# Optimization experiments

Measured on AMD Instinct MI355X. Metric: run time of the kernel, lower is better.

## Reference

```python
import jax, jax.numpy as jnp
import numpy as np

INF = 1e9  # large additive-mask constant (original code's INF)
D_KEY = 64


def setup_inputs() -> dict:
    key = jax.random.key(0)
    kq, kk, kv = jax.random.split(key, 3)
    B, S, D = 8, 2048, 64
    return {
        "query": jax.random.normal(kq, (B, S, D), dtype=jnp.float32),
        "key": jax.random.normal(kk, (B, S, D), dtype=jnp.float32),
        "value": jax.random.normal(kv, (B, S, D), dtype=jnp.float32),
    }


def reference(query, key, value):
    # scores: [B, Sq, Sk]
    scores = jnp.einsum("bqd,bkd->bqk", query, key)
    Sk = key.shape[1]
    # strict upper-triangular additive causal mask, subtracted BEFORE scaling
    tri = jnp.triu(jnp.ones((Sk, Sk), dtype=scores.dtype), k=1) * INF
    scores = scores - tri[None, :, :]
    scale = jnp.asarray(np.sqrt(D_KEY), dtype=scores.dtype)
    attn = jax.nn.softmax(scores / scale, axis=2)  # dropout ratio = 0.0
    return jnp.einsum("bqk,bkd->bqd", attn, value)
```

## Files before the change

### kernel.cpp

```cpp
#include <hip/hip_runtime.h>
#include <hip/hip_bf16.h>

typedef __attribute__((ext_vector_type(8))) short bf16x8;
typedef __attribute__((ext_vector_type(4))) float f32x4;
typedef __attribute__((ext_vector_type(4))) unsigned short us4;

#define BATCH 8
#define SEQ 2048
#define DIM 64
#define QB 64
#define NQT 32
#define NKT 32
#define TE 4096
#define CH 4
#define CPB 144
#define QSCALE (0.125f * 1.44269504088896f)
#define THR 8.0f

__device__ __forceinline__ unsigned short f2bf(float f) {
    return __builtin_bit_cast(unsigned short, __float2bfloat16(f));
}

__device__ __forceinline__ int kswz(int row, int d) {
    return (row * DIM + d) ^ ((row & 7) << 3);
}
__device__ __forceinline__ int vswz(int d, int kv) {
    return (d * 64 + kv) ^ ((((d & 7) ^ ((d >> 2) & 7)) & 7) << 3);
}
__device__ __forceinline__ int pswz(int row, int kv) {
    return (row * 64 + kv) ^ ((row & 7) << 3);
}

#define GLOAD16(gsrc, ldst)                                                     \
    __builtin_amdgcn_global_load_lds(                                           \
        (const __attribute__((address_space(1))) void*)(gsrc),                  \
        (__attribute__((address_space(3))) void*)(ldst), 16, 0, 0)

__global__ __launch_bounds__(256) void prep_kernel(const float* __restrict__ K,
                                                   const float* __restrict__ V,
                                                   unsigned short* __restrict__ Kp,
                                                   unsigned short* __restrict__ Vp) {
    const int batch = blockIdx.x & 7;
    const int t = blockIdx.x >> 3;
    const int tile = batch * NKT + t;
    const int tid = threadIdx.x;
    const float* Kt = K + (size_t)tile * TE;
    const float* Vt = V + (size_t)tile * TE;
    unsigned short* Kd = Kp + (size_t)tile * TE;
    unsigned short* Vd = Vp + (size_t)tile * TE;
    #pragma unroll
    for (int i = 0; i < 4; ++i) {
        int idx = i * 256 + tid;
        int row = idx >> 4;
        int d0 = (idx & 15) << 2;
        f32x4 kf = *(const f32x4*)(Kt + row * DIM + d0);
        us4 kb = {f2bf(kf[0]), f2bf(kf[1]), f2bf(kf[2]), f2bf(kf[3])};
        *(us4*)(&Kd[kswz(row, d0)]) = kb;
    }
    const int dt4 = tid & 15, k4 = tid >> 4;
    f32x4 vf[4];
    #pragma unroll
    for (int rr = 0; rr < 4; ++rr)
        vf[rr] = *(const f32x4*)(Vt + (k4 * 4 + rr) * DIM + dt4 * 4);
    #pragma unroll
    for (int dd = 0; dd < 4; ++dd) {
        us4 vb = {f2bf(vf[0][dd]), f2bf(vf[1][dd]), f2bf(vf[2][dd]), f2bf(vf[3][dd])};
        *(us4*)(&Vd[vswz(dt4 * 4 + dd, k4 * 4)]) = vb;
    }
}

__global__ __launch_bounds__(256, 4) void fa_kernel(const float* __restrict__ Q,
                                                    const unsigned short* __restrict__ Kp,
                                                    const unsigned short* __restrict__ Vp,
                                                    float* __restrict__ PO,
                                                    float* __restrict__ PM,
                                                    float* __restrict__ PL,
                                                    float* __restrict__ O) {
    __shared__ unsigned short KL[2][4096];
    __shared__ unsigned short VL[2][4096];
    __shared__ unsigned short PB[4][1024];

    const int tid = threadIdx.x;
    const int w = tid >> 6, lane = tid & 63, g = lane >> 4, c = lane & 15;

    const int slot = blockIdx.x;
    const int batch = slot & 7;
    const int c0 = (CPB - 1) - (slot >> 3);
    int g2 = 0;
    #pragma unroll
    for (int gg = 1; gg < 8; ++gg) g2 = (c0 >= 2 * gg * (gg + 1)) ? gg : g2;
    const int nc = g2 + 1;
    const int x = c0 - 2 * g2 * nc;
    const int qrow = (x >= nc) + (x >= 2 * nc) + (x >= 3 * nc);
    const int sp = x - qrow * nc;
    const int qi = 4 * g2 + qrow;

    const int q0 = qi * QB;
    const int nt = qi + 1;
    const int t0 = sp * CH;
    const int t1 = (t0 + CH < nt) ? (t0 + CH) : nt;
    const int tiles = t1 - t0;
    const bool dchunk = (t1 == nt);

    const unsigned short* Kb = Kp + (size_t)batch * NKT * TE;
    const unsigned short* Vb = Vp + (size_t)batch * NKT * TE;

#define STAGE_TILE(tidx, buf)                                          \
    do {                                                               \
        const char* Ks_ = (const char*)(Kb + (size_t)(tidx) * TE);     \
        const char* Vs_ = (const char*)(Vb + (size_t)(tidx) * TE);     \
        char* kd_ = (char*)&KL[buf][0];                                \
        char* vd_ = (char*)&VL[buf][0];                                \
        _Pragma("unroll")                                              \
        for (int i_ = 0; i_ < 2; ++i_) {                               \
            int off_ = (w * 2 + i_) * 1024;                            \
            GLOAD16(Ks_ + off_ + lane * 16, kd_ + off_);               \
            GLOAD16(Vs_ + off_ + lane * 16, vd_ + off_);               \
        }                                                              \
    } while (0)

    STAGE_TILE(t0, 0);

    const float* Qrow = Q + (size_t)(batch * SEQ + q0 + w * 16 + c) * DIM;
    f32x4 qf0 = *(const f32x4*)(Qrow + g * 8);
    f32x4 qf1 = *(const f32x4*)(Qrow + g * 8 + 4);
    f32x4 qf2 = *(const f32x4*)(Qrow + 32 + g * 8);
    f32x4 qf3 = *(const f32x4*)(Qrow + 32 + g * 8 + 4);
    bf16x8 qa[2];
    #pragma unroll
    for (int j = 0; j < 4; ++j) {
        qa[0][j]     = (short)f2bf(qf0[j] * QSCALE);
        qa[0][j + 4] = (short)f2bf(qf1[j] * QSCALE);
        qa[1][j]     = (short)f2bf(qf2[j] * QSCALE);
        qa[1][j + 4] = (short)f2bf(qf3[j] * QSCALE);
    }

    float m[4], lsum[4];
    f32x4 o[4];
    #pragma unroll
    for (int r = 0; r < 4; ++r) { m[r] = -1e30f; lsum[r] = 0.f; }
    #pragma unroll
    for (int dt = 0; dt < 4; ++dt) o[dt] = f32x4{0.f, 0.f, 0.f, 0.f};

    __builtin_amdgcn_sched_barrier(0);
    asm volatile("s_waitcnt vmcnt(0)" ::: "memory");
    __builtin_amdgcn_s_barrier();
    __builtin_amdgcn_sched_barrier(0);

    for (int u = 0; u < tiles; ++u) {
        const int cb = u & 1;
        const bool last = (u == tiles - 1);

        if (!last) STAGE_TILE(t0 + u + 1, cb ^ 1);

        f32x4 s[4];
        #pragma unroll
        for (int n = 0; n < 4; ++n) s[n] = f32x4{0.f, 0.f, 0.f, 0.f};
        __builtin_amdgcn_s_setprio(1);
        #pragma unroll
        for (int n = 0; n < 4; ++n)
            #pragma unroll
            for (int f = 0; f < 2; ++f) {
                bf16x8 kb = *(bf16x8*)(&KL[cb][kswz(n * 16 + c, f * 32 + g * 8)]);
                s[n] = __builtin_amdgcn_mfma_f32_16x16x32_bf16(qa[f], kb, s[n], 0, 0, 0);
            }
        __builtin_amdgcn_s_setprio(0);

        if (dchunk && last) {
            const int dbase = (nt - 1) * 64;
            #pragma unroll
            for (int n = 0; n < 4; ++n) {
                int col = dbase + n * 16 + c;
                #pragma unroll
                for (int r = 0; r < 4; ++r)
                    if (col > q0 + w * 16 + g * 4 + r) s[n][r] = -1e30f;
            }
        }

        float pmx[4];
        #pragma unroll
        for (int r = 0; r < 4; ++r)
            pmx[r] = fmaxf(fmaxf(s[0][r], s[1][r]), fmaxf(s[2][r], s[3][r]));
        bool need = false;
        #pragma unroll
        for (int r = 0; r < 4; ++r) need |= (pmx[r] > m[r] + THR);
        if (__any(need)) {
            #pragma unroll
            for (int r = 0; r < 4; ++r) {
                float t2 = pmx[r];
                t2 = fmaxf(t2, __shfl_xor(t2, 1));
                t2 = fmaxf(t2, __shfl_xor(t2, 2));
                t2 = fmaxf(t2, __shfl_xor(t2, 4));
                t2 = fmaxf(t2, __shfl_xor(t2, 8));
                float mn = fmaxf(m[r], t2);
                float alpha = exp2f(m[r] - mn);
                m[r] = mn;
                lsum[r] *= alpha;
                #pragma unroll
                for (int dt = 0; dt < 4; ++dt) o[dt][r] *= alpha;
            }
        }
        #pragma unroll
        for (int n = 0; n < 4; ++n)
            #pragma unroll
            for (int r = 0; r < 4; ++r) {
                float pe = exp2f(s[n][r] - m[r]);
                s[n][r] = pe;
                lsum[r] += pe;
            }

        unsigned short* Pw = &PB[w][0];
        #pragma unroll
        for (int n = 0; n < 4; ++n)
            #pragma unroll
            for (int r = 0; r < 4; ++r)
                Pw[pswz(g * 4 + r, n * 16 + c)] = f2bf(s[n][r]);
        asm volatile("s_waitcnt lgkmcnt(0)" ::: "memory");
        __builtin_amdgcn_sched_barrier(0);

        __builtin_amdgcn_s_setprio(1);
        #pragma unroll
        for (int ks = 0; ks < 2; ++ks) {
            bf16x8 pa = *(bf16x8*)(&Pw[pswz(c, ks * 32 + g * 8)]);
            #pragma unroll
            for (int dt = 0; dt < 4; ++dt) {
                bf16x8 vb = *(bf16x8*)(&VL[cb][vswz(dt * 16 + c, ks * 32 + g * 8)]);
                o[dt] = __builtin_amdgcn_mfma_f32_16x16x32_bf16(pa, vb, o[dt], 0, 0, 0);
            }
        }
        __builtin_amdgcn_s_setprio(0);

        if (!last) {
            __builtin_amdgcn_sched_barrier(0);
            asm volatile("s_waitcnt vmcnt(0)" ::: "memory");
            __builtin_amdgcn_s_barrier();
            __builtin_amdgcn_sched_barrier(0);
        }
    }

    float l[4];
    #pragma unroll
    for (int r = 0; r < 4; ++r) {
        float ts = lsum[r];
        ts += __shfl_xor(ts, 1);
        ts += __shfl_xor(ts, 2);
        ts += __shfl_xor(ts, 4);
        ts += __shfl_xor(ts, 8);
        l[r] = ts;
    }

    if (nt <= CH) {
        #pragma unroll
        for (int r = 0; r < 4; ++r) {
            float inv = 1.f / l[r];
            float* Orow = O + (size_t)(batch * SEQ + q0 + w * 16 + g * 4 + r) * DIM;
            #pragma unroll
            for (int dt = 0; dt < 4; ++dt)
                Orow[dt * 16 + c] = o[dt][r] * inv;
        }
    } else {
        float* Pbase = PO + (size_t)slot * (QB * DIM);
        #pragma unroll
        for (int r = 0; r < 4; ++r) {
            int rowin = w * 16 + g * 4 + r;
            #pragma unroll
            for (int dt = 0; dt < 4; ++dt)
                Pbase[rowin * DIM + dt * 16 + c] = o[dt][r];
            if (c == 0) {
                PM[(size_t)slot * QB + rowin] = m[r];
                PL[(size_t)slot * QB + rowin] = l[r];
            }
        }
    }
#undef STAGE_TILE
}

__global__ __launch_bounds__(256) void combine_kernel(const float* __restrict__ PO,
                                                      const float* __restrict__ PM,
                                                      const float* __restrict__ PL,
                                                      float* __restrict__ O) {
    const int tid = threadIdx.x;
    const int ridx = blockIdx.x * 16 + (tid >> 4);
    const int d0 = (tid & 15) << 2;
    const int batch = ridx / 1792;
    const int rem = ridx - batch * 1792;
    const int qi = 4 + (rem >> 6);
    const int rowin = rem & 63;
    const int a = qi >> 2, b = qi & 3;
    const int nc = a + 1;
    const int pfx = (a + 1) * (2 * a + b);

    float mstar = -1e30f;
    #pragma unroll 4
    for (int sp = 0; sp < nc; ++sp) {
        int sl = ((CPB - 1 - (pfx + sp)) << 3) | batch;
        mstar = fmaxf(mstar, PM[(size_t)sl * QB + rowin]);
    }
    float ls = 0.f;
    f32x4 os = {0.f, 0.f, 0.f, 0.f};
    #pragma unroll 4
    for (int sp = 0; sp < nc; ++sp) {
        int sl = ((CPB - 1 - (pfx + sp)) << 3) | batch;
        float wgt = exp2f(PM[(size_t)sl * QB + rowin] - mstar);
        ls += PL[(size_t)sl * QB + rowin] * wgt;
        f32x4 po = *(const f32x4*)(PO + (size_t)sl * (QB * DIM) + rowin * DIM + d0);
        os += po * wgt;
    }
    const int grow = batch * SEQ + qi * 64 + rowin;
    float inv = 1.f / ls;
    f32x4 res = os * inv;
    *(f32x4*)(O + (size_t)grow * DIM + d0) = res;
}

extern "C" void kernel_launch(void* const* d_in, const int* in_sizes, int n_in,
                              void* d_out, int out_size, void* d_ws, size_t ws_size,
                              hipStream_t stream) {
    const float* Q = (const float*)d_in[0];
    const float* K = (const float*)d_in[1];
    const float* V = (const float*)d_in[2];
    float* O = (float*)d_out;
    (void)in_sizes; (void)n_in; (void)out_size; (void)ws_size;

    const size_t kvelems = (size_t)BATCH * SEQ * DIM;
    unsigned short* Kp = (unsigned short*)d_ws;
    unsigned short* Vp = Kp + kvelems;
    float* PO = (float*)(Vp + kvelems);
    float* PM = PO + (size_t)BATCH * CPB * QB * DIM;
    float* PL = PM + (size_t)BATCH * CPB * QB;

    prep_kernel<<<BATCH * NKT, 256, 0, stream>>>(K, V, Kp, Vp);
    fa_kernel<<<BATCH * CPB, 256, 0, stream>>>(Q, Kp, Vp, PO, PM, PL, O);
    combine_kernel<<<BATCH * 28 * 64 / 16, 256, 0, stream>>>(PO, PM, PL, O);
}
```

Before: 38.39 us.

## Use 128-row query tiles with 8 waves and store bf16 partial outputs

```diff
diff --git a/kernel.cpp b/kernel.cpp
--- a/kernel.cpp
+++ b/kernel.cpp
@@ -8,17 +8,20 @@
 #define BATCH 8
 #define SEQ 2048
 #define DIM 64
-#define QB 64
-#define NQT 32
+#define QB 128
+#define NQT 16
 #define NKT 32
 #define TE 4096
 #define CH 4
-#define CPB 144
+#define CPB 72
 #define QSCALE (0.125f * 1.44269504088896f)
 #define THR 8.0f
 
 __device__ __forceinline__ unsigned short f2bf(float f) {
     return __builtin_bit_cast(unsigned short, __float2bfloat16(f));
+}
+__device__ __forceinline__ float bf2f(unsigned short u) {
+    return __builtin_bit_cast(float, (unsigned)u << 16);
 }
 
 __device__ __forceinline__ int kswz(int row, int d) {
@@ -69,16 +72,16 @@
     }
 }
 
-__global__ __launch_bounds__(256, 4) void fa_kernel(const float* __restrict__ Q,
+__global__ __launch_bounds__(512, 6) void fa_kernel(const float* __restrict__ Q,
                                                     const unsigned short* __restrict__ Kp,
                                                     const unsigned short* __restrict__ Vp,
-                                                    float* __restrict__ PO,
+                                                    unsigned short* __restrict__ PO,
                                                     float* __restrict__ PM,
                                                     float* __restrict__ PL,
                                                     float* __restrict__ O) {
     __shared__ unsigned short KL[2][4096];
     __shared__ unsigned short VL[2][4096];
-    __shared__ unsigned short PB[4][1024];
+    __shared__ unsigned short PB[8][1024];
 
     const int tid = threadIdx.x;
     const int w = tid >> 6, lane = tid & 63, g = lane >> 4, c = lane & 15;
@@ -86,17 +89,19 @@
     const int slot = blockIdx.x;
     const int batch = slot & 7;
     const int c0 = (CPB - 1) - (slot >> 3);
-    int g2 = 0;
-    #pragma unroll
-    for (int gg = 1; gg < 8; ++gg) g2 = (c0 >= 2 * gg * (gg + 1)) ? gg : g2;
-    const int nc = g2 + 1;
-    const int x = c0 - 2 * g2 * nc;
-    const int qrow = (x >= nc) + (x >= 2 * nc) + (x >= 3 * nc);
-    const int sp = x - qrow * nc;
-    const int qi = 4 * g2 + qrow;
-
+    int qi = 0, sp = 0;
+    {
+        int acc = 0;
+        #pragma unroll
+        for (int j = 0; j < NQT; ++j) {
+            int ncj = (j >> 1) + 1;
+            if (c0 >= acc && c0 < acc + ncj) { qi = j; sp = c0 - acc; }
+            acc += ncj;
+        }
+    }
+    const int nc = (qi >> 1) + 1;
     const int q0 = qi * QB;
-    const int nt = qi + 1;
+    const int nt = 2 * qi + 2;
     const int t0 = sp * CH;
     const int t1 = (t0 + CH < nt) ? (t0 + CH) : nt;
     const int tiles = t1 - t0;
@@ -109,14 +114,9 @@
     do {                                                               \
         const char* Ks_ = (const char*)(Kb + (size_t)(tidx) * TE);     \
         const char* Vs_ = (const char*)(Vb + (size_t)(tidx) * TE);     \
-        char* kd_ = (char*)&KL[buf][0];                                \
-        char* vd_ = (char*)&VL[buf][0];                                \
-        _Pragma("unroll")                                              \
-        for (int i_ = 0; i_ < 2; ++i_) {                               \
-            int off_ = (w * 2 + i_) * 1024;                            \
-            GLOAD16(Ks_ + off_ + lane * 16, kd_ + off_);               \
-            GLOAD16(Vs_ + off_ + lane * 16, vd_ + off_);               \
-        }                                                              \
+        int off_ = w * 1024;                                           \
+        GLOAD16(Ks_ + off_ + lane * 16, (char*)&KL[buf][0] + off_);    \
+        GLOAD16(Vs_ + off_ + lane * 16, (char*)&VL[buf][0] + off_);    \
     } while (0)
 
     STAGE_TILE(t0, 0);
@@ -166,8 +166,8 @@
             }
         __builtin_amdgcn_s_setprio(0);
 
-        if (dchunk && last) {
-            const int dbase = (nt - 1) * 64;
+        if (dchunk && u >= tiles - 2) {
+            const int dbase = (t0 + u) * 64;
             #pragma unroll
             for (int n = 0; n < 4; ++n) {
                 int col = dbase + n * 16 + c;
@@ -249,7 +249,7 @@
         l[r] = ts;
     }
 
-    if (nt <= CH) {
+    if (nc == 1) {
         #pragma unroll
         for (int r = 0; r < 4; ++r) {
             float inv = 1.f / l[r];
@@ -259,13 +259,13 @@
                 Orow[dt * 16 + c] = o[dt][r] * inv;
         }
     } else {
-        float* Pbase = PO + (size_t)slot * (QB * DIM);
+        unsigned short* Pbase = PO + (size_t)slot * (QB * DIM);
         #pragma unroll
         for (int r = 0; r < 4; ++r) {
             int rowin = w * 16 + g * 4 + r;
             #pragma unroll
             for (int dt = 0; dt < 4; ++dt)
-                Pbase[rowin * DIM + dt * 16 + c] = o[dt][r];
+                Pbase[rowin * DIM + dt * 16 + c] = f2bf(o[dt][r]);
             if (c == 0) {
                 PM[(size_t)slot * QB + rowin] = m[r];
                 PL[(size_t)slot * QB + rowin] = l[r];
@@ -275,7 +275,7 @@
 #undef STAGE_TILE
 }
 
-__global__ __launch_bounds__(256) void combine_kernel(const float* __restrict__ PO,
+__global__ __launch_bounds__(256) void combine_kernel(const unsigned short* __restrict__ PO,
                                                       const float* __restrict__ PM,
                                                       const float* __restrict__ PL,
                                                       float* __restrict__ O) {
@@ -284,11 +284,11 @@
     const int d0 = (tid & 15) << 2;
     const int batch = ridx / 1792;
     const int rem = ridx - batch * 1792;
-    const int qi = 4 + (rem >> 6);
-    const int rowin = rem & 63;
-    const int a = qi >> 2, b = qi & 3;
+    const int qi = 2 + (rem >> 7);
+    const int rowin = rem & 127;
+    const int a = qi >> 1, b = qi & 1;
     const int nc = a + 1;
-    const int pfx = (a + 1) * (2 * a + b);
+    const int pfx = (a + b) * (a + 1);
 
     float mstar = -1e30f;
     #pragma unroll 4
@@ -303,10 +303,13 @@
         int sl = ((CPB - 1 - (pfx + sp)) << 3) | batch;
         float wgt = exp2f(PM[(size_t)sl * QB + rowin] - mstar);
         ls += PL[(size_t)sl * QB + rowin] * wgt;
-        f32x4 po = *(const f32x4*)(PO + (size_t)sl * (QB * DIM) + rowin * DIM + d0);
-        os += po * wgt;
-    }
-    const int grow = batch * SEQ + qi * 64 + rowin;
+        us4 po = *(const us4*)(PO + (size_t)sl * (QB * DIM) + rowin * DIM + d0);
+        os[0] += bf2f(po[0]) * wgt;
+        os[1] += bf2f(po[1]) * wgt;
+        os[2] += bf2f(po[2]) * wgt;
+        os[3] += bf2f(po[3]) * wgt;
+    }
+    const int grow = batch * SEQ + qi * QB + rowin;
     float inv = 1.f / ls;
     f32x4 res = os * inv;
     *(f32x4*)(O + (size_t)grow * DIM + d0) = res;
@@ -324,11 +327,11 @@
     const size_t kvelems = (size_t)BATCH * SEQ * DIM;
     unsigned short* Kp = (unsigned short*)d_ws;
     unsigned short* Vp = Kp + kvelems;
-    float* PO = (float*)(Vp + kvelems);
-    float* PM = PO + (size_t)BATCH * CPB * QB * DIM;
+    unsigned short* PO = Vp + kvelems;
+    float* PM = (float*)(PO + (size_t)BATCH * CPB * QB * DIM);
     float* PL = PM + (size_t)BATCH * CPB * QB;
 
     prep_kernel<<<BATCH * NKT, 256, 0, stream>>>(K, V, Kp, Vp);
-    fa_kernel<<<BATCH * CPB, 256, 0, stream>>>(Q, Kp, Vp, PO, PM, PL, O);
-    combine_kernel<<<BATCH * 28 * 64 / 16, 256, 0, stream>>>(PO, PM, PL, O);
-}
+    fa_kernel<<<BATCH * CPB, 512, 0, stream>>>(Q, Kp, Vp, PO, PM, PL, O);
+    combine_kernel<<<BATCH * 14 * QB / 16, 256, 0, stream>>>(PO, PM, PL, O);
+}
```

New measurement: 57.03 us. +48.6%, slower.
